# Performance work log

Measured on AMD Instinct MI355X. Metric: run time of the kernel, lower is better.

The kernel has to match this reference:

```python
import jax, jax.numpy as jnp
import numpy as np

ALPHA = 2.0
INF = jnp.float32(1e30)
EPS = jnp.float32(1e-12)


def _pairwise_d2(h, w):
    # Squared Euclidean distance between all pixel pairs of an h x w grid. [N, N]
    yy, xx = jnp.meshgrid(jnp.arange(h), jnp.arange(w), indexing='ij')
    pts = jnp.stack([yy.reshape(-1), xx.reshape(-1)], axis=-1).astype(jnp.float32)  # [N, 2]
    diff = pts[:, None, :] - pts[None, :, :]
    return jnp.sum(diff * diff, axis=-1)


def _edt(mask, d2):
    # scipy.distance_transform_edt semantics: for each pixel, Euclidean distance
    # to the nearest zero (False) pixel. mask: [N] bool, d2: [N, N].
    m = jnp.min(jnp.where(mask[None, :], INF, d2), axis=1)
    return jnp.where(jnp.any(~mask), jnp.sqrt(m), 0.0)


def _distance_field(img, d2):
    # Faithful port of HausdorffDTLoss.distance_field for one 2D image.
    h, w = img.shape
    fg = (img > 0.5).reshape(-1)
    fgd = _edt(fg, d2)            # edt(fg_mask)
    bgd = _edt(~fg, d2)           # edt(bg_mask)
    fg_any = jnp.any(fg)
    bg_any = jnp.any(~fg)
    fmax = jnp.maximum(jnp.max(fgd), EPS)
    bmax = jnp.maximum(jnp.max(bgd), EPS)
    field = (jnp.where(fg_any, fgd / fmax, 0.0)
             + jnp.where(fg_any & bg_any, bgd / bmax, 0.0))
    return field.reshape(h, w)


def setup_inputs() -> dict:
    key = jax.random.key(0)
    k1, k2, k3 = jax.random.split(key, 3)
    R, C, H, W = 128, 80, 28, 28
    preds = jax.random.normal(k1, (R, C, H, W), dtype=jnp.float32)
    targets = jax.random.uniform(k2, (R, H, W), dtype=jnp.float32)
    labels = jax.random.randint(k3, (R,), 0, C)
    return {"preds": preds, "targets": targets, "labels": labels}


def reference(preds, targets, labels):
    R, C, H, W = preds.shape
    d2 = _pairwise_d2(H, W)
    p = jax.nn.sigmoid(preds)
    # pred = preds[i][labels[i]]  -> gather the per-ROI class channel
    p_sel = jnp.take_along_axis(p, labels[:, None, None, None], axis=1)[:, 0]  # [R, H, W]
    df = lambda im: _distance_field(im, d2)
    preds_dt = jax.vmap(df)(p_sel)      # [R, H, W]
    targets_dt = jax.vmap(df)(targets)  # [R, H, W]
    dist = preds_dt ** ALPHA + targets_dt ** ALPHA
    # torch loop accumulates `distance` across samples without resetting -> cumsum
    cum = jnp.cumsum(dist, axis=0)
    err = (p_sel - targets) ** 2
    hd_loss = jnp.sum(jnp.mean(err * cum, axis=(1, 2))) / R
    return hd_loss
```

## Files before the change

### kernel.cpp

```cpp
#include <hip/hip_runtime.h>

#define R 128
#define C 80
#define HH 28
#define WW 28
#define NPIX 784
#define BIGD (1 << 26)

__global__ __launch_bounds__(256) void edt_field_kernel(
    const float* __restrict__ preds,
    const float* __restrict__ targets,
    const int* __restrict__ labels,
    float* __restrict__ distP,
    float* __restrict__ distT,
    float* __restrict__ p_sel,
    float* __restrict__ out)
{
    __shared__ unsigned fgrow[HH];
    __shared__ int rowd[2][HH][WW];
    __shared__ int md2[NPIX];
    __shared__ int redF[256], redB[256];
    __shared__ float invF, invB;
    __shared__ int s_uniform;

    const int tid = threadIdx.x;
    const int b = blockIdx.x;

    if (b == 0 && tid == 0) out[0] = 0.0f;

    if (tid < HH) fgrow[tid] = 0u;
    __syncthreads();

    const bool isPred = (b < R);
    const float* src;
    float* pstore = nullptr;
    if (isPred) {
        const int lab = labels[b];
        src = preds + ((size_t)b * C + (size_t)lab) * NPIX;
        pstore = p_sel + (size_t)b * NPIX;
    } else {
        src = targets + (size_t)(b - R) * NPIX;
    }

    for (int j = tid; j < NPIX; j += 256) {
        float v = src[j];
        float s;
        if (isPred) {
            s = 1.0f / (1.0f + expf(-v));
            pstore[j] = s;
        } else {
            s = v;
        }
        if (s > 0.5f) {
            atomicOr(&fgrow[j / WW], 1u << (j % WW));
        }
    }
    __syncthreads();

    for (int e = tid; e < 2 * NPIX; e += 256) {
        const int c = (e >= NPIX);
        const int rem = e - c * NPIX;
        const int r = rem / WW;
        const int x = rem - r * WW;
        const unsigned fr = fgrow[r];
        const unsigned w = c ? fr : (~fr & 0x0FFFFFFFu);
        int dv;
        if (w == 0u) {
            dv = BIGD;
        } else {
            const unsigned wl = w & ((2u << x) - 1u);
            const unsigned wr = w >> x;
            const int dl = wl ? (x - (31 - __builtin_clz(wl))) : 10000;
            const int dr = wr ? __builtin_ctz(wr) : 10000;
            const int d = dl < dr ? dl : dr;
            dv = d * d;
        }
        rowd[c][r][x] = dv;
    }
    __syncthreads();

    int localF = -1, localB = -1;
    for (int j = tid; j < NPIX; j += 256) {
        const int y = j / WW;
        const int x = j - y * WW;
        const int c = (fgrow[y] >> x) & 1;
        const int* rd = &rowd[c ^ 1][0][x];
        int m = 0x3FFFFFFF;
        #pragma unroll
        for (int r = 0; r < HH; ++r) {
            const int dy = y - r;
            const int cand = dy * dy + rd[r * WW];
            m = cand < m ? cand : m;
        }
        md2[j] = m;
        if (c) localF = m > localF ? m : localF;
        else   localB = m > localB ? m : localB;
    }
    redF[tid] = localF;
    redB[tid] = localB;
    __syncthreads();
    for (int s = 128; s > 0; s >>= 1) {
        if (tid < s) {
            redF[tid] = redF[tid + s] > redF[tid] ? redF[tid + s] : redF[tid];
            redB[tid] = redB[tid + s] > redB[tid] ? redB[tid + s] : redB[tid];
        }
        __syncthreads();
    }
    if (tid == 0) {
        const int mF = redF[0], mB = redB[0];
        if (mF < 0 || mB < 0) {
            s_uniform = 1; invF = 0.0f; invB = 0.0f;
        } else {
            s_uniform = 0;
            invF = 1.0f / (float)mF;
            invB = 1.0f / (float)mB;
        }
    }
    __syncthreads();

    float* dst = isPred ? (distP + (size_t)b * NPIX)
                        : (distT + (size_t)(b - R) * NPIX);
    const int uni = s_uniform;
    for (int j = tid; j < NPIX; j += 256) {
        float fsq = 0.0f;
        if (!uni) {
            const int y = j / WW;
            const int x = j - y * WW;
            const int c = (fgrow[y] >> x) & 1;
            fsq = (float)md2[j] * (c ? invF : invB);
        }
        dst[j] = fsq;
    }
}

__global__ __launch_bounds__(64) void reduce_kernel(
    const float* __restrict__ distP,
    const float* __restrict__ distT,
    const float* __restrict__ p_sel,
    const float* __restrict__ targets,
    float* __restrict__ out)
{
    const int px = blockIdx.x * 64 + threadIdx.x;
    float acc = 0.0f;
    if (px < NPIX) {
        float cum = 0.0f;
        for (int i = 0; i < R; ++i) {
            const size_t o = (size_t)i * NPIX + px;
            cum += distP[o] + distT[o];
            const float e = p_sel[o] - targets[o];
            acc += e * e * cum;
        }
    }
    #pragma unroll
    for (int off = 32; off > 0; off >>= 1)
        acc += __shfl_down(acc, off, 64);
    if (threadIdx.x == 0)
        atomicAdd(out, acc * (1.0f / ((float)R * (float)NPIX)));
}

extern "C" void kernel_launch(void* const* d_in, const int* in_sizes, int n_in,
                              void* d_out, int out_size, void* d_ws, size_t ws_size,
                              hipStream_t stream) {
    const float* preds = (const float*)d_in[0];
    const float* targets = (const float*)d_in[1];
    const int* labels = (const int*)d_in[2];
    float* out = (float*)d_out;

    float* ws = (float*)d_ws;
    float* distP = ws;
    float* distT = ws + (size_t)R * NPIX;
    float* p_sel = ws + (size_t)2 * R * NPIX;

    hipLaunchKernelGGL(edt_field_kernel, dim3(2 * R), dim3(256), 0, stream,
                       preds, targets, labels, distP, distT, p_sel, out);
    hipLaunchKernelGGL(reduce_kernel, dim3((NPIX + 63) / 64), dim3(64), 0, stream,
                       distP, distT, p_sel, targets, out);
}
```

Before: 92.90 us.

## Transpose intermediates and parallelize cumulative sum with per-pixel warp scan

The EDT kernel now writes distance fields and squared error in pixel-major (transposed) layout, computing the squared error in place instead of storing p_sel. The reduction becomes one block per pixel that does a shuffle-based prefix scan over the 128 ROIs, replacing the serial 128-step loop in only 13 blocks. This is meant to remove the latency-bound serial cumsum and the low parallelism of the reduce. The cost is strided, uncoalesced writes in the first kernel and 784 atomics on the output.

Result: no change. 92.39 us (-0.5%).

```diff
diff --git a/kernel.cpp b/kernel.cpp
--- a/kernel.cpp
+++ b/kernel.cpp
@@ -11,9 +11,9 @@
     const float* __restrict__ preds,
     const float* __restrict__ targets,
     const int* __restrict__ labels,
-    float* __restrict__ distP,
-    float* __restrict__ distT,
-    float* __restrict__ p_sel,
+    float* __restrict__ distP_t,
+    float* __restrict__ distT_t,
+    float* __restrict__ err_t,
     float* __restrict__ out)
 {
     __shared__ unsigned fgrow[HH];
@@ -32,14 +32,14 @@
     __syncthreads();
 
     const bool isPred = (b < R);
+    const int rb = isPred ? b : (b - R);
     const float* src;
-    float* pstore = nullptr;
+    const float* tgt = targets + (size_t)rb * NPIX;
     if (isPred) {
         const int lab = labels[b];
         src = preds + ((size_t)b * C + (size_t)lab) * NPIX;
-        pstore = p_sel + (size_t)b * NPIX;
     } else {
-        src = targets + (size_t)(b - R) * NPIX;
+        src = tgt;
     }
 
     for (int j = tid; j < NPIX; j += 256) {
@@ -47,7 +47,8 @@
         float s;
         if (isPred) {
             s = 1.0f / (1.0f + expf(-v));
-            pstore[j] = s;
+            const float e = s - tgt[j];
+            err_t[(size_t)j * R + b] = e * e;
         } else {
             s = v;
         }
@@ -118,8 +119,7 @@
     }
     __syncthreads();
 
-    float* dst = isPred ? (distP + (size_t)b * NPIX)
-                        : (distT + (size_t)(b - R) * NPIX);
+    float* dst = isPred ? distP_t : distT_t;
     const int uni = s_uniform;
     for (int j = tid; j < NPIX; j += 256) {
         float fsq = 0.0f;
@@ -129,33 +129,43 @@
             const int c = (fgrow[y] >> x) & 1;
             fsq = (float)md2[j] * (c ? invF : invB);
         }
-        dst[j] = fsq;
+        dst[(size_t)j * R + rb] = fsq;
     }
 }
 
-__global__ __launch_bounds__(64) void reduce_kernel(
-    const float* __restrict__ distP,
-    const float* __restrict__ distT,
-    const float* __restrict__ p_sel,
-    const float* __restrict__ targets,
+__global__ __launch_bounds__(128) void scan_reduce_kernel(
+    const float* __restrict__ distP_t,
+    const float* __restrict__ distT_t,
+    const float* __restrict__ err_t,
     float* __restrict__ out)
 {
-    const int px = blockIdx.x * 64 + threadIdx.x;
-    float acc = 0.0f;
-    if (px < NPIX) {
-        float cum = 0.0f;
-        for (int i = 0; i < R; ++i) {
-            const size_t o = (size_t)i * NPIX + px;
-            cum += distP[o] + distT[o];
-            const float e = p_sel[o] - targets[o];
-            acc += e * e * cum;
-        }
+    __shared__ float wsum;
+    __shared__ float bacc[2];
+
+    const int px = blockIdx.x;
+    const int i = threadIdx.x;
+    const size_t o = (size_t)px * R + i;
+
+    float cum = distP_t[o] + distT_t[o];
+    const float e2 = err_t[o];
+
+    #pragma unroll
+    for (int off = 1; off < 64; off <<= 1) {
+        const float v = __shfl_up(cum, off, 64);
+        if ((i & 63) >= off) cum += v;
     }
+    if (i == 63) wsum = cum;
+    __syncthreads();
+    if (i >= 64) cum += wsum;
+
+    float acc = e2 * cum;
     #pragma unroll
     for (int off = 32; off > 0; off >>= 1)
         acc += __shfl_down(acc, off, 64);
-    if (threadIdx.x == 0)
-        atomicAdd(out, acc * (1.0f / ((float)R * (float)NPIX)));
+    if ((i & 63) == 0) bacc[i >> 6] = acc;
+    __syncthreads();
+    if (i == 0)
+        atomicAdd(out, (bacc[0] + bacc[1]) * (1.0f / ((float)R * (float)NPIX)));
 }
 
 extern "C" void kernel_launch(void* const* d_in, const int* in_sizes, int n_in,
@@ -167,12 +177,12 @@
     float* out = (float*)d_out;
 
     float* ws = (float*)d_ws;
-    float* distP = ws;
-    float* distT = ws + (size_t)R * NPIX;
-    float* p_sel = ws + (size_t)2 * R * NPIX;
+    float* distP_t = ws;
+    float* distT_t = ws + (size_t)R * NPIX;
+    float* err_t   = ws + (size_t)2 * R * NPIX;
 
     hipLaunchKernelGGL(edt_field_kernel, dim3(2 * R), dim3(256), 0, stream,
-                       preds, targets, labels, distP, distT, p_sel, out);
-    hipLaunchKernelGGL(reduce_kernel, dim3((NPIX + 63) / 64), dim3(64), 0, stream,
-                       distP, distT, p_sel, targets, out);
+                       preds, targets, labels, distP_t, distT_t, err_t, out);
+    hipLaunchKernelGGL(scan_reduce_kernel, dim3(NPIX), dim3(128), 0, stream,
+                       distP_t, distT_t, err_t, out);
 }
```
